# Optimization experiments

Measured on AMD Instinct MI355X. Metric: run time of the kernel, lower is better.

## Reference

```python
import jax, jax.numpy as jnp
import numpy as np

NUM_TAG = 128
T, B = 1024, 512


def setup_inputs() -> dict:
    key = jax.random.key(0)
    k_em, k_tag, k_s, k_t, k_e = jax.random.split(key, 5)
    emissions = jax.random.normal(k_em, (T, B, NUM_TAG), dtype=jnp.float32)
    tags = jax.random.randint(k_tag, (T, B), 0, NUM_TAG, dtype=jnp.int32)
    mask = jnp.ones((T, B), dtype=jnp.float32)
    # parameters: uniform(-0.1, 0.1) as in reset_params
    start_transitions = jax.random.uniform(k_s, (NUM_TAG,), minval=-0.1, maxval=0.1, dtype=jnp.float32)
    transitions = jax.random.uniform(k_t, (NUM_TAG, NUM_TAG), minval=-0.1, maxval=0.1, dtype=jnp.float32)
    end_transitions = jax.random.uniform(k_e, (NUM_TAG,), minval=-0.1, maxval=0.1, dtype=jnp.float32)
    return {
        "emissions": emissions,
        "tags": tags,
        "mask": mask,
        "start_transitions": start_transitions,
        "transitions": transitions,
        "end_transitions": end_transitions,
    }


def _path_score(emissions, tags, mask, start_transitions, transitions, end_transitions):
    # emissions: [T,B,K], tags/mask: [T,B]
    b_idx = jnp.arange(tags.shape[1])
    # emission score of the gold tag at each step: [T,B]
    em_tag = jnp.take_along_axis(emissions, tags[:, :, None].astype(jnp.int32), axis=2)[:, :, 0]
    scores = start_transitions[tags[0]] + (em_tag * mask).sum(axis=0)
    # transition scores along the gold path, masked: [T-1,B]
    scores = scores + (transitions[tags[:-1], tags[1:]] * mask[1:]).sum(axis=0)
    last_idx = mask.astype(jnp.int32).sum(axis=0) - 1  # [B]
    last_tag = tags[last_idx, b_idx]
    return scores + end_transitions[last_tag]


def _log_partition(emissions, mask, start_transitions, transitions, end_transitions):
    log_prob0 = start_transitions[None, :] + emissions[0]  # [B,K]

    def step(log_prob, xs):
        em_t, m_t = xs  # [B,K], [B]
        # score[b,i,j] = log_prob[b,i] + transitions[i,j] + em_t[b,j]
        score = jax.nn.logsumexp(
            log_prob[:, :, None] + transitions[None, :, :] + em_t[:, None, :], axis=1
        )
        new_lp = score * m_t[:, None] + log_prob * (1.0 - m_t)[:, None]
        return new_lp, None

    log_prob, _ = jax.lax.scan(step, log_prob0, (emissions[1:], mask[1:]))
    return jax.nn.logsumexp(log_prob + end_transitions[None, :], axis=1)  # [B]


def reference(emissions, tags, mask, start_transitions, transitions, end_transitions):
    path = _path_score(emissions, tags, mask, start_transitions, transitions, end_transitions)
    log_z = _log_partition(emissions, mask, start_transitions, transitions, end_transitions)
    return (path - log_z).sum()
```

## Files before the change

kernel.cpp:

```cpp
#include <hip/hip_runtime.h>
#include <cstdint>

#define TT 1024
#define BB 512
#define KK 128

typedef __attribute__((ext_vector_type(8))) short short8;
typedef __attribute__((ext_vector_type(4))) float f4;
typedef __attribute__((ext_vector_type(4))) unsigned int uint4v;

__device__ __forceinline__ unsigned short f2bf_rtne(float x) {
  unsigned u = __float_as_uint(x);
  u += 0x7FFF + ((u >> 16) & 1);
  return (unsigned short)(u >> 16);
}

__device__ __forceinline__ unsigned pack_trunc(float l, float h) {
  return __builtin_amdgcn_perm(__float_as_uint(h), __float_as_uint(l), 0x07060302u);
}

__global__ __launch_bounds__(64, 1) void crf_forward(
    const float* __restrict__ em, const float* __restrict__ mask,
    const float* __restrict__ start_t, const float* __restrict__ trans,
    const float* __restrict__ end_t, float* __restrict__ logz)
{
  const int lane = threadIdx.x & 63;
  const int q    = lane >> 4;
  const int lo   = lane & 15;
  const int b0   = blockIdx.x * 16;

  const size_t TS = (size_t)BB * KK;
  const float* emlane = em + (size_t)(b0 + lo) * KK + 4 * q;
  const float* mrow   = mask + (b0 + lo);

  short8 Af[8][4];
#pragma unroll
  for (int mt = 0; mt < 8; ++mt)
#pragma unroll
    for (int kt = 0; kt < 4; ++kt) {
      short8 v;
#pragma unroll
      for (int j = 0; j < 8; ++j) {
        const int ck = 32 * kt + 16 * (j >> 2) + 4 * q + (j & 3);
        v[j] = (short)f2bf_rtne(__expf(trans[(size_t)ck * KK + 16 * mt + lo]));
      }
      Af[mt][kt] = v;
    }

  f4 S[8];
  uint4v PB[4];
  float base = 0.f, mvPrev = 1.0f;
#pragma unroll
  for (int mt = 0; mt < 8; ++mt) {
    const f4 e0 = *(const f4*)(emlane + 16 * mt);
    const f4 st = *(const f4*)(start_t + 16 * mt + 4 * q);
#pragma unroll
    for (int i = 0; i < 4; ++i) S[mt][i] = __expf(st[i] + e0[i]);
  }
#pragma unroll
  for (int kt = 0; kt < 4; ++kt) {
    PB[kt][0] = pack_trunc(S[2 * kt][0],     S[2 * kt][1]);
    PB[kt][1] = pack_trunc(S[2 * kt][2],     S[2 * kt][3]);
    PB[kt][2] = pack_trunc(S[2 * kt + 1][0], S[2 * kt + 1][1]);
    PB[kt][3] = pack_trunc(S[2 * kt + 1][2], S[2 * kt + 1][3]);
  }

  f4 bufA[8], bufB[8];
  float mkA, mkB;
#pragma unroll
  for (int mt = 0; mt < 8; ++mt) {
    bufB[mt] = *(const f4*)(emlane + 1 * TS + 16 * mt);
    bufA[mt] = *(const f4*)(emlane + 2 * TS + 16 * mt);
  }
  mkB = mrow[1 * BB];
  mkA = mrow[2 * BB];

  auto STEP = [&](const int t, f4 (&bufC)[8], float& mkC) {
    const float mk = mkC;
    float ps = 1.0f, kln2 = 0.f;
    const bool scale_step = ((t & 3) == 1) && (t > 1);
    if (scale_step) {
      const int k = (int)(__float_as_uint(mvPrev) >> 23) - 127;
      ps = __uint_as_float((unsigned)(127 - k) << 23);
      kln2 = (float)k * 0.6931471805599453f;
    }

    f4 X[8];
#pragma unroll
    for (int mt = 0; mt < 8; ++mt) {
      f4 x;
#pragma unroll
      for (int i = 0; i < 4; ++i) x[i] = __expf(bufC[mt][i]);
      if (scale_step) x *= ps;
      X[mt] = x;
    }

    const int tp = (t + 2 < TT) ? (t + 2) : (TT - 1);
    const float* p = emlane + (size_t)tp * TS;
#pragma unroll
    for (int mt = 0; mt < 8; ++mt) bufC[mt] = *(const f4*)(p + 16 * mt);
    mkC = mrow[(size_t)tp * BB];

    short8 Bf[4];
#pragma unroll
    for (int kt = 0; kt < 4; ++kt) Bf[kt] = __builtin_bit_cast(short8, PB[kt]);

    f4 acc[8];
#pragma unroll
    for (int mt = 0; mt < 8; ++mt) acc[mt] = f4{0.f, 0.f, 0.f, 0.f};
#pragma unroll
    for (int kt = 0; kt < 4; ++kt)
#pragma unroll
      for (int mt = 0; mt < 8; ++mt)
        acc[mt] = __builtin_amdgcn_mfma_f32_16x16x32_bf16(Af[mt][kt], Bf[kt], acc[mt], 0, 0, 0);

    const bool upd = (mk != 0.f);
#pragma unroll
    for (int mt = 0; mt < 8; ++mt)
#pragma unroll
      for (int i = 0; i < 4; ++i) {
        const float n = acc[mt][i] * X[mt][i];
        S[mt][i] = upd ? n : S[mt][i];
      }
    if (scale_step && upd) base += kln2;

#pragma unroll
    for (int kt = 0; kt < 4; ++kt) {
      PB[kt][0] = pack_trunc(S[2 * kt][0],     S[2 * kt][1]);
      PB[kt][1] = pack_trunc(S[2 * kt][2],     S[2 * kt][3]);
      PB[kt][2] = pack_trunc(S[2 * kt + 1][0], S[2 * kt + 1][1]);
      PB[kt][3] = pack_trunc(S[2 * kt + 1][2], S[2 * kt + 1][3]);
    }

    if ((t & 3) == 0) {
      float mv = S[0][0];
#pragma unroll
      for (int mt = 0; mt < 8; ++mt)
#pragma unroll
        for (int i = 0; i < 4; ++i) mv = fmaxf(mv, S[mt][i]);
      mv = fmaxf(mv, __shfl_xor(mv, 16));
      mv = fmaxf(mv, __shfl_xor(mv, 32));
      mvPrev = mv;
    }
  };

  for (int t = 1; t + 1 < TT; t += 2) {
    STEP(t, bufB, mkB);
    STEP(t + 1, bufA, mkA);
  }
  STEP(TT - 1, bufB, mkB);

  {
    float s = 0.f;
#pragma unroll
    for (int mt = 0; mt < 8; ++mt) {
      const f4 ed = *(const f4*)(end_t + 16 * mt + 4 * q);
#pragma unroll
      for (int i = 0; i < 4; ++i) s += S[mt][i] * __expf(ed[i]);
    }
    s += __shfl_xor(s, 16);
    s += __shfl_xor(s, 32);
    if (q == 0) logz[b0 + lo] = base + logf(s);
  }
}

__global__ __launch_bounds__(512) void crf_path_tb(
    const float* __restrict__ em, const int* __restrict__ tags,
    const float* __restrict__ mask, const float* __restrict__ trans,
    float* __restrict__ ws_tb)
{
  const int t = blockIdx.x, b = threadIdx.x;
  const int tg = tags[t * BB + b];
  const float mk = mask[t * BB + b];
  float v = em[((size_t)t * BB + b) * KK + tg] * mk;
  if (t >= 1) {
    const int tgp = tags[(t - 1) * BB + b];
    v += trans[(size_t)tgp * KK + tg] * mk;
  }
  __shared__ float red[8];
#pragma unroll
  for (int off = 32; off; off >>= 1) v += __shfl_xor(v, off);
  if ((b & 63) == 0) red[b >> 6] = v;
  __syncthreads();
  if (b == 0) {
    float s = 0.f;
#pragma unroll
    for (int i = 0; i < 8; ++i) s += red[i];
    ws_tb[t] = s;
  }
}

__global__ __launch_bounds__(64) void crf_bterm(
    const int* __restrict__ tags, const float* __restrict__ mask,
    const float* __restrict__ start_t, const float* __restrict__ end_t,
    float* __restrict__ ws_bt)
{
  const int b = blockIdx.x, tid = threadIdx.x;
  float ms = 0.f;
  for (int t = tid; t < TT; t += 64) ms += mask[t * BB + b];
#pragma unroll
  for (int off = 32; off; off >>= 1) ms += __shfl_xor(ms, off);
  if (tid == 0) {
    const int last = (int)(ms + 0.5f) - 1;
    ws_bt[b] = start_t[tags[b]] + end_t[tags[(size_t)last * BB + b]];
  }
}

__global__ __launch_bounds__(1024) void crf_final(
    const float* __restrict__ ws_tb, const float* __restrict__ ws_bt,
    const float* __restrict__ ws_lz, float* __restrict__ out)
{
  const int tid = threadIdx.x;
  float v = ws_tb[tid];
  if (tid < BB) v += ws_bt[tid] - ws_lz[tid];
  __shared__ float red[16];
#pragma unroll
  for (int off = 32; off; off >>= 1) v += __shfl_xor(v, off);
  if ((tid & 63) == 0) red[tid >> 6] = v;
  __syncthreads();
  if (tid == 0) {
    float s = 0.f;
#pragma unroll
    for (int i = 0; i < 16; ++i) s += red[i];
    out[0] = s;
  }
}

extern "C" void kernel_launch(void* const* d_in, const int* in_sizes, int n_in,
                              void* d_out, int out_size, void* d_ws, size_t ws_size,
                              hipStream_t stream) {
  (void)in_sizes; (void)n_in; (void)out_size; (void)ws_size;
  const float* em    = (const float*)d_in[0];
  const int*   tags  = (const int*)  d_in[1];
  const float* mask  = (const float*)d_in[2];
  const float* st    = (const float*)d_in[3];
  const float* trans = (const float*)d_in[4];
  const float* et    = (const float*)d_in[5];
  float* out = (float*)d_out;

  float* ws_tb = (float*)d_ws;
  float* ws_bt = ws_tb + 1024;
  float* ws_lz = ws_bt + 512;

  crf_path_tb<<<TT, 512, 0, stream>>>(em, tags, mask, trans, ws_tb);
  crf_bterm  <<<BB, 64, 0, stream>>>(tags, mask, st, et, ws_bt);
  crf_forward<<<32, 64, 0, stream>>>(em, mask, st, trans, et, ws_lz);
  crf_final  <<<1, 1024, 0, stream>>>(ws_tb, ws_bt, ws_lz, out);
}
```

Baseline: 1.236 ms.

## Split CRF forward into producer/consumer waves with LDS ring buffer

```diff
diff --git a/kernel.cpp b/kernel.cpp
--- a/kernel.cpp
+++ b/kernel.cpp
@@ -4,6 +4,8 @@
 #define TT 1024
 #define BB 512
 #define KK 128
+#define XPAD 132
+#define NSLOT 8
 
 typedef __attribute__((ext_vector_type(8))) short short8;
 typedef __attribute__((ext_vector_type(4))) float f4;
@@ -19,111 +21,59 @@
   return __builtin_amdgcn_perm(__float_as_uint(h), __float_as_uint(l), 0x07060302u);
 }
 
-__global__ __launch_bounds__(64, 1) void crf_forward(
+__device__ __forceinline__ void lgkm_barrier() {
+  __atomic_signal_fence(__ATOMIC_SEQ_CST);
+  __builtin_amdgcn_s_waitcnt(0xC07F);
+  __builtin_amdgcn_s_barrier();
+  __atomic_signal_fence(__ATOMIC_SEQ_CST);
+}
+
+__global__ __launch_bounds__(128, 1) void crf_forward(
     const float* __restrict__ em, const float* __restrict__ mask,
     const float* __restrict__ start_t, const float* __restrict__ trans,
     const float* __restrict__ end_t, float* __restrict__ logz)
 {
-  const int lane = threadIdx.x & 63;
+  const int tid  = threadIdx.x;
+  const int wid  = tid >> 6;
+  const int lane = tid & 63;
   const int q    = lane >> 4;
   const int lo   = lane & 15;
   const int b0   = blockIdx.x * 16;
 
+  __shared__ __align__(16) float Xs[NSLOT][16][XPAD];
+
   const size_t TS = (size_t)BB * KK;
   const float* emlane = em + (size_t)(b0 + lo) * KK + 4 * q;
   const float* mrow   = mask + (b0 + lo);
 
   short8 Af[8][4];
-#pragma unroll
-  for (int mt = 0; mt < 8; ++mt)
-#pragma unroll
-    for (int kt = 0; kt < 4; ++kt) {
-      short8 v;
-#pragma unroll
-      for (int j = 0; j < 8; ++j) {
-        const int ck = 32 * kt + 16 * (j >> 2) + 4 * q + (j & 3);
-        v[j] = (short)f2bf_rtne(__expf(trans[(size_t)ck * KK + 16 * mt + lo]));
-      }
-      Af[mt][kt] = v;
-    }
-
   f4 S[8];
   uint4v PB[4];
   float base = 0.f, mvPrev = 1.0f;
-#pragma unroll
-  for (int mt = 0; mt < 8; ++mt) {
-    const f4 e0 = *(const f4*)(emlane + 16 * mt);
-    const f4 st = *(const f4*)(start_t + 16 * mt + 4 * q);
-#pragma unroll
-    for (int i = 0; i < 4; ++i) S[mt][i] = __expf(st[i] + e0[i]);
-  }
-#pragma unroll
-  for (int kt = 0; kt < 4; ++kt) {
-    PB[kt][0] = pack_trunc(S[2 * kt][0],     S[2 * kt][1]);
-    PB[kt][1] = pack_trunc(S[2 * kt][2],     S[2 * kt][3]);
-    PB[kt][2] = pack_trunc(S[2 * kt + 1][0], S[2 * kt + 1][1]);
-    PB[kt][3] = pack_trunc(S[2 * kt + 1][2], S[2 * kt + 1][3]);
-  }
-
-  f4 bufA[8], bufB[8];
-  float mkA, mkB;
-#pragma unroll
-  for (int mt = 0; mt < 8; ++mt) {
-    bufB[mt] = *(const f4*)(emlane + 1 * TS + 16 * mt);
-    bufA[mt] = *(const f4*)(emlane + 2 * TS + 16 * mt);
-  }
-  mkB = mrow[1 * BB];
-  mkA = mrow[2 * BB];
-
-  auto STEP = [&](const int t, f4 (&bufC)[8], float& mkC) {
-    const float mk = mkC;
-    float ps = 1.0f, kln2 = 0.f;
-    const bool scale_step = ((t & 3) == 1) && (t > 1);
-    if (scale_step) {
-      const int k = (int)(__float_as_uint(mvPrev) >> 23) - 127;
-      ps = __uint_as_float((unsigned)(127 - k) << 23);
-      kln2 = (float)k * 0.6931471805599453f;
-    }
-
-    f4 X[8];
-#pragma unroll
-    for (int mt = 0; mt < 8; ++mt) {
-      f4 x;
-#pragma unroll
-      for (int i = 0; i < 4; ++i) x[i] = __expf(bufC[mt][i]);
-      if (scale_step) x *= ps;
-      X[mt] = x;
-    }
-
-    const int tp = (t + 2 < TT) ? (t + 2) : (TT - 1);
-    const float* p = emlane + (size_t)tp * TS;
-#pragma unroll
-    for (int mt = 0; mt < 8; ++mt) bufC[mt] = *(const f4*)(p + 16 * mt);
-    mkC = mrow[(size_t)tp * BB];
-
-    short8 Bf[4];
-#pragma unroll
-    for (int kt = 0; kt < 4; ++kt) Bf[kt] = __builtin_bit_cast(short8, PB[kt]);
-
-    f4 acc[8];
-#pragma unroll
-    for (int mt = 0; mt < 8; ++mt) acc[mt] = f4{0.f, 0.f, 0.f, 0.f};
-#pragma unroll
-    for (int kt = 0; kt < 4; ++kt)
-#pragma unroll
-      for (int mt = 0; mt < 8; ++mt)
-        acc[mt] = __builtin_amdgcn_mfma_f32_16x16x32_bf16(Af[mt][kt], Bf[kt], acc[mt], 0, 0, 0);
-
-    const bool upd = (mk != 0.f);
+
+  f4 LA[8], LB[8], LC[8], LD[8];
+  float mA = 0.f, mB = 0.f, mC = 0.f, mD = 0.f;
+
+  if (wid == 0) {
 #pragma unroll
     for (int mt = 0; mt < 8; ++mt)
 #pragma unroll
-      for (int i = 0; i < 4; ++i) {
-        const float n = acc[mt][i] * X[mt][i];
-        S[mt][i] = upd ? n : S[mt][i];
+      for (int kt = 0; kt < 4; ++kt) {
+        short8 v;
+#pragma unroll
+        for (int j = 0; j < 8; ++j) {
+          const int ck = 32 * kt + 16 * (j >> 2) + 4 * q + (j & 3);
+          v[j] = (short)f2bf_rtne(__expf(trans[(size_t)ck * KK + 16 * mt + lo]));
+        }
+        Af[mt][kt] = v;
       }
-    if (scale_step && upd) base += kln2;
-
+#pragma unroll
+    for (int mt = 0; mt < 8; ++mt) {
+      const f4 e0 = *(const f4*)(emlane + 16 * mt);
+      const f4 st = *(const f4*)(start_t + 16 * mt + 4 * q);
+#pragma unroll
+      for (int i = 0; i < 4; ++i) S[mt][i] = __expf(st[i] + e0[i]);
+    }
 #pragma unroll
     for (int kt = 0; kt < 4; ++kt) {
       PB[kt][0] = pack_trunc(S[2 * kt][0],     S[2 * kt][1]);
@@ -131,8 +81,82 @@
       PB[kt][2] = pack_trunc(S[2 * kt + 1][0], S[2 * kt + 1][1]);
       PB[kt][3] = pack_trunc(S[2 * kt + 1][2], S[2 * kt + 1][3]);
     }
-
-    if ((t & 3) == 0) {
+  } else {
+#pragma unroll
+    for (int mt = 0; mt < 8; ++mt) {
+      LA[mt] = *(const f4*)(emlane + 1 * TS + 16 * mt);
+      LB[mt] = *(const f4*)(emlane + 2 * TS + 16 * mt);
+      LC[mt] = *(const f4*)(emlane + 3 * TS + 16 * mt);
+      LD[mt] = *(const f4*)(emlane + 4 * TS + 16 * mt);
+    }
+    mA = mrow[1 * BB]; mB = mrow[2 * BB]; mC = mrow[3 * BB]; mD = mrow[4 * BB];
+  }
+
+  auto PROD = [&](const int t, f4 (&Ls)[8], float& ms) {
+    if (t > TT) return;
+    float* xb = &Xs[t & 7][lo][0];
+#pragma unroll
+    for (int mt = 0; mt < 8; ++mt) {
+      f4 x;
+#pragma unroll
+      for (int i = 0; i < 4; ++i) x[i] = __expf(Ls[mt][i]);
+      *(f4*)(xb + 16 * mt + 4 * q) = x;
+    }
+    if (q == 0) xb[128] = (t <= TT - 1) ? ms : 0.f;
+    const int tp = (t + 4 <= TT - 1) ? (t + 4) : (TT - 1);
+#pragma unroll
+    for (int mt = 0; mt < 8; ++mt)
+      Ls[mt] = *(const f4*)(emlane + (size_t)tp * TS + 16 * mt);
+    ms = mrow[(size_t)tp * BB];
+  };
+
+  auto CONS = [&](const int t, const bool scale_cand, const bool do_renorm) {
+    const float* xb = &Xs[t & 7][lo][0];
+    f4 X[8];
+#pragma unroll
+    for (int mt = 0; mt < 8; ++mt) X[mt] = *(const f4*)(xb + 16 * mt + 4 * q);
+    const float mk = xb[128];
+
+    float ps = 1.0f, kln2 = 0.f;
+    if (scale_cand) {
+      const int k = (int)(__float_as_uint(mvPrev) >> 23) - 127;
+      ps = __uint_as_float((unsigned)(127 - k) << 23);
+      kln2 = (float)k * 0.6931471805599453f;
+    }
+
+    short8 Bf[4];
+#pragma unroll
+    for (int kt = 0; kt < 4; ++kt) Bf[kt] = __builtin_bit_cast(short8, PB[kt]);
+
+    f4 acc[8];
+#pragma unroll
+    for (int mt = 0; mt < 8; ++mt) acc[mt] = f4{0.f, 0.f, 0.f, 0.f};
+#pragma unroll
+    for (int kt = 0; kt < 4; ++kt)
+#pragma unroll
+      for (int mt = 0; mt < 8; ++mt)
+        acc[mt] = __builtin_amdgcn_mfma_f32_16x16x32_bf16(Af[mt][kt], Bf[kt], acc[mt], 0, 0, 0);
+
+    const bool upd = (mk != 0.f);
+#pragma unroll
+    for (int mt = 0; mt < 8; ++mt)
+#pragma unroll
+      for (int i = 0; i < 4; ++i) {
+        float n = acc[mt][i] * X[mt][i];
+        if (scale_cand) n *= ps;
+        S[mt][i] = upd ? n : S[mt][i];
+      }
+    if (scale_cand && upd) base += kln2;
+
+#pragma unroll
+    for (int kt = 0; kt < 4; ++kt) {
+      PB[kt][0] = pack_trunc(S[2 * kt][0],     S[2 * kt][1]);
+      PB[kt][1] = pack_trunc(S[2 * kt][2],     S[2 * kt][3]);
+      PB[kt][2] = pack_trunc(S[2 * kt + 1][0], S[2 * kt + 1][1]);
+      PB[kt][3] = pack_trunc(S[2 * kt + 1][2], S[2 * kt + 1][3]);
+    }
+
+    if (do_renorm) {
       float mv = S[0][0];
 #pragma unroll
       for (int mt = 0; mt < 8; ++mt)
@@ -144,13 +168,32 @@
     }
   };
 
-  for (int t = 1; t + 1 < TT; t += 2) {
-    STEP(t, bufB, mkB);
-    STEP(t + 1, bufA, mkA);
-  }
-  STEP(TT - 1, bufB, mkB);
-
-  {
+  if (wid == 1) { PROD(1, LA, mA); PROD(2, LB, mB); PROD(3, LC, mC); PROD(4, LD, mD); }
+  lgkm_barrier();
+
+  if (wid == 0) {
+    CONS(1, false, false); CONS(2, false, false);
+    CONS(3, false, false); CONS(4, false, true);
+  } else {
+    PROD(5, LA, mA); PROD(6, LB, mB); PROD(7, LC, mC); PROD(8, LD, mD);
+  }
+  lgkm_barrier();
+
+  for (int g = 1; g < 256; ++g) {
+    const int t0 = 4 * g;
+    if (wid == 0) {
+      CONS(t0 + 1, true,  false);
+      CONS(t0 + 2, false, false);
+      CONS(t0 + 3, false, false);
+      CONS(t0 + 4, false, true);
+    } else {
+      PROD(t0 + 5, LA, mA); PROD(t0 + 6, LB, mB);
+      PROD(t0 + 7, LC, mC); PROD(t0 + 8, LD, mD);
+    }
+    lgkm_barrier();
+  }
+
+  if (wid == 0) {
     float s = 0.f;
 #pragma unroll
     for (int mt = 0; mt < 8; ++mt) {
@@ -244,6 +287,6 @@
 
   crf_path_tb<<<TT, 512, 0, stream>>>(em, tags, mask, trans, ws_tb);
   crf_bterm  <<<BB, 64, 0, stream>>>(tags, mask, st, et, ws_bt);
-  crf_forward<<<32, 64, 0, stream>>>(em, mask, st, trans, et, ws_lz);
+  crf_forward<<<32, 128, 0, stream>>>(em, mask, st, trans, et, ws_lz);
   crf_final  <<<1, 1024, 0, stream>>>(ws_tb, ws_bt, ws_lz, out);
 }
```

New measurement: 1.164 ms. 5.8% less time.
